# Kernel optimization log

Measured on AMD Instinct MI355X. Metric: run time of the kernel, lower is better.

## Reference

```python
import jax, jax.numpy as jnp
import numpy as np

D_MODEL, N_HEADS = 512, 8
HEAD_DIM = D_MODEL // N_HEADS
LN_EPS = 1e-5


def setup_inputs() -> dict:
    key = jax.random.key(0)
    ks = jax.random.split(key, 6)
    b, n = 8, 1024
    x = jax.random.normal(ks[0], (b, n, D_MODEL), dtype=jnp.float32)
    W_qkv = jax.random.normal(ks[1], (D_MODEL, 3 * D_MODEL), dtype=jnp.float32) * (1.0 / np.sqrt(D_MODEL))
    b_qkv = jnp.zeros((3 * D_MODEL,), dtype=jnp.float32)
    reattn_w = jax.random.normal(ks[2], (N_HEADS, N_HEADS), dtype=jnp.float32)
    ln_g = jnp.ones((N_HEADS,), dtype=jnp.float32)
    ln_b = jnp.zeros((N_HEADS,), dtype=jnp.float32)
    W_out = jax.random.normal(ks[3], (D_MODEL, D_MODEL), dtype=jnp.float32) * (1.0 / np.sqrt(D_MODEL))
    b_out = jnp.zeros((D_MODEL,), dtype=jnp.float32)
    return {"x": x, "W_qkv": W_qkv, "b_qkv": b_qkv, "reattn_w": reattn_w,
            "ln_g": ln_g, "ln_b": ln_b, "W_out": W_out, "b_out": b_out}


def reference(x, W_qkv, b_qkv, reattn_w, ln_g, ln_b, W_out, b_out):
    b, n, _ = x.shape
    scale = jnp.float32(HEAD_DIM ** -0.5)  # lsa=False -> non-trainable constant
    qkv = x @ W_qkv + b_qkv                                  # (b, n, 3*d_model)
    q, k, v = jnp.split(qkv, 3, axis=-1)
    def to_heads(t):  # b n (h d) -> b h n d
        return t.reshape(b, n, N_HEADS, HEAD_DIM).transpose(0, 2, 1, 3)
    q, k, v = to_heads(q), to_heads(k), to_heads(v)
    scores = jnp.einsum('bhid,bhjd->bhij', q, k) * scale      # (b, h, n, n)
    attn = jax.nn.softmax(scores, axis=-1)
    # cross-head re-attention mix
    attn = jnp.einsum('bhij,hk->bkij', attn, reattn_w)
    # LayerNorm over the head axis (axis=1)
    mu = jnp.mean(attn, axis=1, keepdims=True)
    var = jnp.var(attn, axis=1, keepdims=True)
    attn = (attn - mu) * jax.lax.rsqrt(var + LN_EPS)
    attn = attn * ln_g[None, :, None, None] + ln_b[None, :, None, None]
    out = jnp.einsum('bhij,bhjd->bhid', attn, v)              # (b, h, n, d)
    out = out.transpose(0, 2, 1, 3).reshape(b, n, D_MODEL)    # b n (h d)
    out = out @ W_out + b_out
    return (out, attn)
```

## Files before the change

### kernel.cpp

```cpp
#include <hip/hip_runtime.h>
#include <hip/hip_bf16.h>

#define SCALE_ 0.125f
#define LN_EPS_ 1e-5f

typedef __attribute__((ext_vector_type(8))) short bf16x8;
typedef __attribute__((ext_vector_type(4))) float f32x4;

__device__ __forceinline__ ushort f2b(float f) {
  union { float f; unsigned u; } x; x.f = f;
  unsigned r = x.u + 0x7FFFu + ((x.u >> 16) & 1u);
  return (ushort)(r >> 16);
}
__device__ __forceinline__ unsigned cvtpk(float lo, float hi) {
  union { __hip_bfloat162 h; unsigned u; } x;
  x.h = __float22bfloat162_rn(make_float2(lo, hi));
  return x.u;
}

__device__ __forceinline__ f32x4 mfma16(bf16x8 a, bf16x8 b, f32x4 c) {
  return __builtin_amdgcn_mfma_f32_16x16x32_bf16(a, b, c, 0, 0, 0);
}

__device__ __forceinline__ void bar_lds() {
  asm volatile("s_waitcnt lgkmcnt(0)\n\ts_barrier" ::: "memory");
  __builtin_amdgcn_sched_barrier(0);
}

__global__ __launch_bounds__(256) void cast_transpose2(const float* __restrict__ srcA,
                                                       ushort* __restrict__ dstA,
                                                       const float* __restrict__ srcB,
                                                       ushort* __restrict__ dstB) {
  __shared__ ushort t[64][65];
  const int bid = blockIdx.x;
  const float* src;
  ushort* dst;
  int R, C, c0, r0;
  if (bid < 192) {
    src = srcA; dst = dstA; R = 512; C = 1536;
    c0 = (bid % 24) * 64; r0 = (bid / 24) * 64;
  } else {
    src = srcB; dst = dstB; R = 512; C = 512;
    int b2 = bid - 192;
    c0 = (b2 % 8) * 64; r0 = (b2 / 8) * 64;
  }
  const int tid = threadIdx.x;
  const int lr = tid >> 2, lc = (tid & 3) * 16;
#pragma unroll
  for (int u = 0; u < 4; ++u) {
    float4 v = *(const float4*)&src[(size_t)(r0 + lr) * C + c0 + lc + u * 4];
    t[lc + u * 4 + 0][lr] = f2b(v.x);
    t[lc + u * 4 + 1][lr] = f2b(v.y);
    t[lc + u * 4 + 2][lr] = f2b(v.z);
    t[lc + u * 4 + 3][lr] = f2b(v.w);
  }
  __syncthreads();
#pragma unroll
  for (int u = 0; u < 2; ++u) {
    bf16x8 o;
#pragma unroll
    for (int e = 0; e < 8; ++e) o[e] = (short)t[lr][lc + u * 8 + e];
    *(bf16x8*)&dst[(size_t)(c0 + lr) * R + r0 + lc + u * 8] = o;
  }
}

__global__ __launch_bounds__(256) void qkv_mfma(const float* __restrict__ x,
                                                const ushort* __restrict__ Wt,
                                                const float* __restrict__ bias,
                                                ushort* __restrict__ q,
                                                ushort* __restrict__ k,
                                                ushort* __restrict__ vt) {
  __shared__ ushort A[128][40];
  __shared__ ushort Bs[128][40];
  const int tid = threadIdx.x;
  const int bid = blockIdx.x;
  const int obid = (bid & 7) * 96 + (bid >> 3);
  const int n0 = (obid % 12) * 128;
  const int m0 = (obid / 12) * 128;
  const int lane = tid & 63, wid = tid >> 6;
  const int wr = wid >> 1, wc = wid & 1;
  const int lr = lane & 15, g4 = lane >> 4;
  const int sr = tid >> 1, sco = (tid & 1) * 16;
  f32x4 acc[4][4] = {};
  for (int k0 = 0; k0 < 512; k0 += 32) {
    {
      const float4* xs = (const float4*)&x[(size_t)(m0 + sr) * 512 + k0 + sco];
      float4 v0 = xs[0], v1 = xs[1], v2 = xs[2], v3 = xs[3];
      bf16x8 p0, p1;
      p0[0] = (short)f2b(v0.x); p0[1] = (short)f2b(v0.y);
      p0[2] = (short)f2b(v0.z); p0[3] = (short)f2b(v0.w);
      p0[4] = (short)f2b(v1.x); p0[5] = (short)f2b(v1.y);
      p0[6] = (short)f2b(v1.z); p0[7] = (short)f2b(v1.w);
      p1[0] = (short)f2b(v2.x); p1[1] = (short)f2b(v2.y);
      p1[2] = (short)f2b(v2.z); p1[3] = (short)f2b(v2.w);
      p1[4] = (short)f2b(v3.x); p1[5] = (short)f2b(v3.y);
      p1[6] = (short)f2b(v3.z); p1[7] = (short)f2b(v3.w);
      *(bf16x8*)&A[sr][sco] = p0;
      *(bf16x8*)&A[sr][sco + 8] = p1;
    }
    {
      const bf16x8* wp = (const bf16x8*)&Wt[(size_t)(n0 + sr) * 512 + k0 + sco];
      *(bf16x8*)&Bs[sr][sco] = wp[0];
      *(bf16x8*)&Bs[sr][sco + 8] = wp[1];
    }
    __syncthreads();
    bf16x8 af[4], bf[4];
#pragma unroll
    for (int mr = 0; mr < 4; ++mr) af[mr] = *(bf16x8*)&A[wr * 64 + mr * 16 + lr][g4 * 8];
#pragma unroll
    for (int nr = 0; nr < 4; ++nr) bf[nr] = *(bf16x8*)&Bs[wc * 64 + nr * 16 + lr][g4 * 8];
#pragma unroll
    for (int mr = 0; mr < 4; ++mr)
#pragma unroll
      for (int nr = 0; nr < 4; ++nr) acc[mr][nr] = mfma16(af[mr], bf[nr], acc[mr][nr]);
    __syncthreads();
  }
  const int part = n0 >> 9;
#pragma unroll
  for (int mr = 0; mr < 4; ++mr)
#pragma unroll
    for (int nr = 0; nr < 4; ++nr) {
      const int n = n0 + wc * 64 + nr * 16 + lr;
      const int h = (n & 511) >> 6, d = n & 63;
      const float bb = bias[n];
#pragma unroll
      for (int r = 0; r < 4; ++r) {
        int token = m0 + wr * 64 + mr * 16 + g4 * 4 + r;
        int bi = token >> 10, ii = token & 1023;
        ushort valb = f2b(acc[mr][nr][r] + bb);
        if (part == 0)
          q[(((size_t)(bi * 8 + h) * 1024 + ii) * 64) + d] = valb;
        else if (part == 1)
          k[(((size_t)(bi * 8 + h) * 1024 + ii) * 64) + d] = valb;
        else
          vt[((size_t)(bi * 8 + h) * 64 + d) * 1024 + ii] = valb;
      }
    }
}

__global__ __launch_bounds__(512, 2) void attn_fused(const ushort* __restrict__ q,
                                                     const ushort* __restrict__ k,
                                                     const ushort* __restrict__ vt,
                                                     const float* __restrict__ rw,
                                                     const float* __restrict__ ln_g,
                                                     const float* __restrict__ ln_b,
                                                     float* __restrict__ attn,
                                                     ushort* __restrict__ pv) {
  __shared__ float PM[8][32][36];
  __shared__ float wsh[64];
  __shared__ float gsh[8], bsh[8];

  const int tid = threadIdx.x;
  const int lane = tid & 63;
  const int h = tid >> 6;
  const int obid = ((blockIdx.x & 7) << 5) + (blockIdx.x >> 3);
  const int i0 = (obid & 31) * 32;
  const int b = obid >> 5;
  const int lr = lane & 15, g4 = lane >> 4;

  const int bh = b * 8 + h;
  const ushort* qh = q + ((size_t)bh * 1024 + i0) * 64;
  const ushort* kh = k + (size_t)bh * 65536;
  const ushort* vth = vt + (size_t)bh * 65536;

  if (tid < 64) wsh[tid] = rw[tid];
  if (tid < 8) { gsh[tid] = ln_g[tid]; bsh[tid] = ln_b[tid]; }

  bf16x8 qf[2][2];
#pragma unroll
  for (int ir = 0; ir < 2; ++ir)
#pragma unroll
    for (int ks = 0; ks < 2; ++ks)
      qf[ir][ks] = *(const bf16x8*)&qh[(size_t)(ir * 16 + lr) * 64 + ks * 32 + g4 * 8];

  float psum[2] = {0.f, 0.f};
  {
    bf16x8 kc[4], kn[4];
#pragma unroll
    for (int jr = 0; jr < 2; ++jr)
#pragma unroll
      for (int ks = 0; ks < 2; ++ks)
        kc[jr * 2 + ks] = *(const bf16x8*)&kh[(size_t)(jr * 16 + lr) * 64 + ks * 32 + g4 * 8];
    for (int jt = 0; jt < 32; ++jt) {
      const int j0n = ((jt + 1) & 31) * 32;
#pragma unroll
      for (int jr = 0; jr < 2; ++jr)
#pragma unroll
        for (int ks = 0; ks < 2; ++ks)
          kn[jr * 2 + ks] =
              *(const bf16x8*)&kh[(size_t)(j0n + jr * 16 + lr) * 64 + ks * 32 + g4 * 8];
      f32x4 sa[2][2] = {};
#pragma unroll
      for (int jr = 0; jr < 2; ++jr)
#pragma unroll
        for (int ir = 0; ir < 2; ++ir) {
          sa[jr][ir] = mfma16(kc[jr * 2 + 0], qf[ir][0], sa[jr][ir]);
          sa[jr][ir] = mfma16(kc[jr * 2 + 1], qf[ir][1], sa[jr][ir]);
        }
#pragma unroll
      for (int jr = 0; jr < 2; ++jr)
#pragma unroll
        for (int ir = 0; ir < 2; ++ir)
#pragma unroll
          for (int r = 0; r < 4; ++r) psum[ir] += __expf(sa[jr][ir][r] * SCALE_);
#pragma unroll
      for (int i = 0; i < 4; ++i) kc[i] = kn[i];
    }
  }
  float inv_[2];
#pragma unroll
  for (int ir = 0; ir < 2; ++ir) {
    float s = psum[ir];
    s += __shfl_xor(s, 16);
    s += __shfl_xor(s, 32);
    inv_[ir] = 1.0f / s;
  }

  f32x4 oaccT[4][2] = {};
  const int pair = tid & 1, chunk = tid >> 1;
  const int m_ii = chunk >> 3, m_jj = (chunk & 7) * 4;
  const int k2base = pair * 4;

  bf16x8 kc[4], kn[4];
#pragma unroll
  for (int jr = 0; jr < 2; ++jr)
#pragma unroll
    for (int ks = 0; ks < 2; ++ks)
      kc[jr * 2 + ks] = *(const bf16x8*)&kh[(size_t)(jr * 16 + lr) * 64 + ks * 32 + g4 * 8];

  for (int jt = 0; jt < 32; ++jt) {
    const int j0 = jt * 32;
    const int j0n = ((jt + 1) & 31) * 32;
#pragma unroll
    for (int jr = 0; jr < 2; ++jr)
#pragma unroll
      for (int ks = 0; ks < 2; ++ks)
        kn[jr * 2 + ks] =
            *(const bf16x8*)&kh[(size_t)(j0n + jr * 16 + lr) * 64 + ks * 32 + g4 * 8];

    f32x4 sa[2][2] = {};
#pragma unroll
    for (int jr = 0; jr < 2; ++jr)
#pragma unroll
      for (int ir = 0; ir < 2; ++ir) {
        sa[jr][ir] = mfma16(kc[jr * 2 + 0], qf[ir][0], sa[jr][ir]);
        sa[jr][ir] = mfma16(kc[jr * 2 + 1], qf[ir][1], sa[jr][ir]);
      }
#pragma unroll
    for (int jr = 0; jr < 2; ++jr)
#pragma unroll
      for (int ir = 0; ir < 2; ++ir) {
        f32x4 pw;
#pragma unroll
        for (int r = 0; r < 4; ++r) pw[r] = __expf(sa[jr][ir][r] * SCALE_) * inv_[ir];
        *(f32x4*)&PM[h][ir * 16 + lr][jr * 16 + g4 * 4] = pw;
      }

    bf16x8 vc[4];
#pragma unroll
    for (int dr = 0; dr < 4; ++dr)
      vc[dr] = *(const bf16x8*)&vth[(size_t)(dr * 16 + lr) * 1024 + j0 + g4 * 8];

    bar_lds();

    float4 ph[8];
#pragma unroll
    for (int h2 = 0; h2 < 8; ++h2) ph[h2] = *(const float4*)&PM[h2][m_ii][m_jj];
    float mixed[4][4];
#pragma unroll
    for (int k2l = 0; k2l < 4; ++k2l) {
      float a0 = 0.f, a1 = 0.f, a2 = 0.f, a3 = 0.f;
#pragma unroll
      for (int h2 = 0; h2 < 8; ++h2) {
        float w = wsh[h2 * 8 + k2base + k2l];
        a0 += ph[h2].x * w; a1 += ph[h2].y * w;
        a2 += ph[h2].z * w; a3 += ph[h2].w * w;
      }
      mixed[k2l][0] = a0; mixed[k2l][1] = a1; mixed[k2l][2] = a2; mixed[k2l][3] = a3;
    }
    float mu[4], rs_[4];
#pragma unroll
    for (int e = 0; e < 4; ++e) {
      float mp = mixed[0][e] + mixed[1][e] + mixed[2][e] + mixed[3][e];
      mu[e] = (mp + __shfl_xor(mp, 1)) * 0.125f;
    }
#pragma unroll
    for (int e = 0; e < 4; ++e) {
      float vp = 0.f;
#pragma unroll
      for (int k2l = 0; k2l < 4; ++k2l) {
        float d = mixed[k2l][e] - mu[e];
        vp += d * d;
      }
      float var = (vp + __shfl_xor(vp, 1)) * 0.125f;
      rs_[e] = rsqrtf(var + LN_EPS_);
    }
#pragma unroll
    for (int k2l = 0; k2l < 4; ++k2l) {
      int k2 = k2base + k2l;
      float g = gsh[k2], be = bsh[k2];
      f32x4 o;
      o[0] = (mixed[k2l][0] - mu[0]) * rs_[0] * g + be;
      o[1] = (mixed[k2l][1] - mu[1]) * rs_[1] * g + be;
      o[2] = (mixed[k2l][2] - mu[2]) * rs_[2] * g + be;
      o[3] = (mixed[k2l][3] - mu[3]) * rs_[3] * g + be;
      __builtin_nontemporal_store(
          o, (f32x4*)&attn[((size_t)(b * 8 + k2) << 20) + ((size_t)(i0 + m_ii) << 10) +
                           j0 + m_jj]);
      *(f32x4*)&PM[k2][m_ii][m_jj] = o;
    }

    bar_lds();

    bf16x8 pab[2];
#pragma unroll
    for (int ic = 0; ic < 2; ++ic) {
      const float* pr = &PM[h][ic * 16 + lr][g4 * 8];
      float4 p0 = *(const float4*)&pr[0];
      float4 p1 = *(const float4*)&pr[4];
      union { bf16x8 v; unsigned u[4]; } pk;
      pk.u[0] = cvtpk(p0.x, p0.y);
      pk.u[1] = cvtpk(p0.z, p0.w);
      pk.u[2] = cvtpk(p1.x, p1.y);
      pk.u[3] = cvtpk(p1.z, p1.w);
      pab[ic] = pk.v;
    }
#pragma unroll
    for (int dr = 0; dr < 4; ++dr) {
      oaccT[dr][0] = mfma16(vc[dr], pab[0], oaccT[dr][0]);
      oaccT[dr][1] = mfma16(vc[dr], pab[1], oaccT[dr][1]);
    }

#pragma unroll
    for (int i = 0; i < 4; ++i) kc[i] = kn[i];
  }

  ushort* po = pv + ((size_t)bh * 1024 + i0) * 64;
#pragma unroll
  for (int ic = 0; ic < 2; ++ic)
#pragma unroll
    for (int dr = 0; dr < 4; ++dr) {
      union { ushort4 s; unsigned u[2]; } o;
      o.u[0] = cvtpk(oaccT[dr][ic][0], oaccT[dr][ic][1]);
      o.u[1] = cvtpk(oaccT[dr][ic][2], oaccT[dr][ic][3]);
      *(ushort4*)&po[(size_t)(ic * 16 + lr) * 64 + dr * 16 + g4 * 4] = o.s;
    }
}

__global__ __launch_bounds__(256) void out_mfma(const ushort* __restrict__ pvb,
                                                const ushort* __restrict__ Wt,
                                                const float* __restrict__ bias,
                                                float* __restrict__ out) {
  __shared__ ushort A[128][40];
  __shared__ ushort Bs[128][40];
  const int tid = threadIdx.x;
  const int bid = blockIdx.x;
  const int obid = ((bid & 7) << 5) + (bid >> 3);
  const int n0 = (obid & 3) * 128;
  const int m0 = (obid >> 2) * 128;
  const int lane = tid & 63, wid = tid >> 6;
  const int wr = wid >> 1, wc = wid & 1;
  const int lr = lane & 15, g4 = lane >> 4;
  const int sr = tid >> 1, sco = (tid & 1) * 16;
  f32x4 acc[4][4] = {};
  for (int k0 = 0; k0 < 512; k0 += 32) {
    {
      int token = m0 + sr;
      int bi = token >> 10, ii = token & 1023;
      int f = k0 + sco;
      int hh = f >> 6, d = f & 63;
      const bf16x8* src =
          (const bf16x8*)&pvb[(((size_t)(bi * 8 + hh)) * 1024 + ii) * 64 + d];
      *(bf16x8*)&A[sr][sco] = src[0];
      *(bf16x8*)&A[sr][sco + 8] = src[1];
    }
    {
      const bf16x8* wp = (const bf16x8*)&Wt[(size_t)(n0 + sr) * 512 + k0 + sco];
      *(bf16x8*)&Bs[sr][sco] = wp[0];
      *(bf16x8*)&Bs[sr][sco + 8] = wp[1];
    }
    __syncthreads();
    bf16x8 af[4], bf[4];
#pragma unroll
    for (int mr = 0; mr < 4; ++mr) af[mr] = *(bf16x8*)&A[wr * 64 + mr * 16 + lr][g4 * 8];
#pragma unroll
    for (int nr = 0; nr < 4; ++nr) bf[nr] = *(bf16x8*)&Bs[wc * 64 + nr * 16 + lr][g4 * 8];
#pragma unroll
    for (int mr = 0; mr < 4; ++mr)
#pragma unroll
      for (int nr = 0; nr < 4; ++nr) acc[mr][nr] = mfma16(af[mr], bf[nr], acc[mr][nr]);
    __syncthreads();
  }
#pragma unroll
  for (int mr = 0; mr < 4; ++mr)
#pragma unroll
    for (int nr = 0; nr < 4; ++nr) {
      const int n = n0 + wc * 64 + nr * 16 + lr;
      const float bb = bias[n];
#pragma unroll
      for (int r = 0; r < 4; ++r) {
        int token = m0 + wr * 64 + mr * 16 + g4 * 4 + r;
        out[(size_t)token * 512 + n] = acc[mr][nr][r] + bb;
      }
    }
}

extern "C" void kernel_launch(void* const* d_in, const int* in_sizes, int n_in,
                              void* d_out, int out_size, void* d_ws, size_t ws_size,
                              hipStream_t stream) {
  const float* x    = (const float*)d_in[0];
  const float* Wqkv = (const float*)d_in[1];
  const float* bqkv = (const float*)d_in[2];
  const float* rw   = (const float*)d_in[3];
  const float* lng  = (const float*)d_in[4];
  const float* lnb  = (const float*)d_in[5];
  const float* Wout = (const float*)d_in[6];
  const float* bout = (const float*)d_in[7];

  float* out  = (float*)d_out;
  float* attn = (float*)d_out + 4194304;

  char* wsb = (char*)d_ws;
  ushort* q     = (ushort*)(wsb);
  ushort* k     = (ushort*)(wsb + (8u << 20));
  ushort* vt    = (ushort*)(wsb + (16u << 20));
  ushort* pvb   = (ushort*)(wsb + (24u << 20));
  ushort* Wqkvt = (ushort*)(wsb + (32u << 20));
  ushort* Woutt = (ushort*)(wsb + (33u << 20) + (1u << 19));

  cast_transpose2<<<dim3(256), 256, 0, stream>>>(Wqkv, Wqkvt, Wout, Woutt);
  qkv_mfma<<<dim3(768), 256, 0, stream>>>(x, Wqkvt, bqkv, q, k, vt);
  attn_fused<<<dim3(256), 512, 0, stream>>>(q, k, vt, rw, lng, lnb, attn, pvb);
  out_mfma<<<dim3(256), 256, 0, stream>>>(pvb, Woutt, bout, out);
}
```

Before: 170.7 us.

## Split attention into denominator kernel and single-wave cross-head attn_pv kernel

```diff
diff --git a/kernel.cpp b/kernel.cpp
--- a/kernel.cpp
+++ b/kernel.cpp
@@ -20,11 +20,6 @@
 
 __device__ __forceinline__ f32x4 mfma16(bf16x8 a, bf16x8 b, f32x4 c) {
   return __builtin_amdgcn_mfma_f32_16x16x32_bf16(a, b, c, 0, 0, 0);
-}
-
-__device__ __forceinline__ void bar_lds() {
-  asm volatile("s_waitcnt lgkmcnt(0)\n\ts_barrier" ::: "memory");
-  __builtin_amdgcn_sched_barrier(0);
 }
 
 __global__ __launch_bounds__(256) void cast_transpose2(const float* __restrict__ srcA,
@@ -138,33 +133,17 @@
     }
 }
 
-__global__ __launch_bounds__(512, 2) void attn_fused(const ushort* __restrict__ q,
-                                                     const ushort* __restrict__ k,
-                                                     const ushort* __restrict__ vt,
-                                                     const float* __restrict__ rw,
-                                                     const float* __restrict__ ln_g,
-                                                     const float* __restrict__ ln_b,
-                                                     float* __restrict__ attn,
-                                                     ushort* __restrict__ pv) {
-  __shared__ float PM[8][32][36];
-  __shared__ float wsh[64];
-  __shared__ float gsh[8], bsh[8];
-
-  const int tid = threadIdx.x;
-  const int lane = tid & 63;
-  const int h = tid >> 6;
-  const int obid = ((blockIdx.x & 7) << 5) + (blockIdx.x >> 3);
-  const int i0 = (obid & 31) * 32;
-  const int b = obid >> 5;
+__global__ __launch_bounds__(64) void denoms(const ushort* __restrict__ q,
+                                             const ushort* __restrict__ k,
+                                             float* __restrict__ invg) {
+  const int bid = blockIdx.x;
+  const int obid = ((bid & 7) << 8) + (bid >> 3);
+  const int bh = obid >> 5;
+  const int it = obid & 31;
+  const int lane = threadIdx.x;
   const int lr = lane & 15, g4 = lane >> 4;
-
-  const int bh = b * 8 + h;
-  const ushort* qh = q + ((size_t)bh * 1024 + i0) * 64;
+  const ushort* qh = q + ((size_t)bh * 1024 + it * 32) * 64;
   const ushort* kh = k + (size_t)bh * 65536;
-  const ushort* vth = vt + (size_t)bh * 65536;
-
-  if (tid < 64) wsh[tid] = rw[tid];
-  if (tid < 8) { gsh[tid] = ln_g[tid]; bsh[tid] = ln_b[tid]; }
 
   bf16x8 qf[2][2];
 #pragma unroll
@@ -174,177 +153,165 @@
       qf[ir][ks] = *(const bf16x8*)&qh[(size_t)(ir * 16 + lr) * 64 + ks * 32 + g4 * 8];
 
   float psum[2] = {0.f, 0.f};
-  {
-    bf16x8 kc[4], kn[4];
+  bf16x8 kc[4], kn[4];
+#pragma unroll
+  for (int jr = 0; jr < 2; ++jr)
+#pragma unroll
+    for (int ks = 0; ks < 2; ++ks)
+      kc[jr * 2 + ks] = *(const bf16x8*)&kh[(size_t)(jr * 16 + lr) * 64 + ks * 32 + g4 * 8];
+  for (int jt = 0; jt < 32; ++jt) {
+    const int j0n = ((jt + 1) & 31) * 32;
 #pragma unroll
     for (int jr = 0; jr < 2; ++jr)
 #pragma unroll
       for (int ks = 0; ks < 2; ++ks)
-        kc[jr * 2 + ks] = *(const bf16x8*)&kh[(size_t)(jr * 16 + lr) * 64 + ks * 32 + g4 * 8];
-    for (int jt = 0; jt < 32; ++jt) {
-      const int j0n = ((jt + 1) & 31) * 32;
-#pragma unroll
-      for (int jr = 0; jr < 2; ++jr)
-#pragma unroll
-        for (int ks = 0; ks < 2; ++ks)
-          kn[jr * 2 + ks] =
-              *(const bf16x8*)&kh[(size_t)(j0n + jr * 16 + lr) * 64 + ks * 32 + g4 * 8];
-      f32x4 sa[2][2] = {};
-#pragma unroll
-      for (int jr = 0; jr < 2; ++jr)
-#pragma unroll
-        for (int ir = 0; ir < 2; ++ir) {
-          sa[jr][ir] = mfma16(kc[jr * 2 + 0], qf[ir][0], sa[jr][ir]);
-          sa[jr][ir] = mfma16(kc[jr * 2 + 1], qf[ir][1], sa[jr][ir]);
-        }
-#pragma unroll
-      for (int jr = 0; jr < 2; ++jr)
-#pragma unroll
-        for (int ir = 0; ir < 2; ++ir)
-#pragma unroll
-          for (int r = 0; r < 4; ++r) psum[ir] += __expf(sa[jr][ir][r] * SCALE_);
-#pragma unroll
-      for (int i = 0; i < 4; ++i) kc[i] = kn[i];
-    }
-  }
-  float inv_[2];
+        kn[jr * 2 + ks] =
+            *(const bf16x8*)&kh[(size_t)(j0n + jr * 16 + lr) * 64 + ks * 32 + g4 * 8];
+    f32x4 sa[2][2] = {};
+#pragma unroll
+    for (int jr = 0; jr < 2; ++jr)
+#pragma unroll
+      for (int ir = 0; ir < 2; ++ir) {
+        sa[jr][ir] = mfma16(kc[jr * 2 + 0], qf[ir][0], sa[jr][ir]);
+        sa[jr][ir] = mfma16(kc[jr * 2 + 1], qf[ir][1], sa[jr][ir]);
+      }
+#pragma unroll
+    for (int jr = 0; jr < 2; ++jr)
+#pragma unroll
+      for (int ir = 0; ir < 2; ++ir)
+#pragma unroll
+        for (int r = 0; r < 4; ++r) psum[ir] += __expf(sa[jr][ir][r] * SCALE_);
+#pragma unroll
+    for (int i = 0; i < 4; ++i) kc[i] = kn[i];
+  }
 #pragma unroll
   for (int ir = 0; ir < 2; ++ir) {
     float s = psum[ir];
     s += __shfl_xor(s, 16);
     s += __shfl_xor(s, 32);
-    inv_[ir] = 1.0f / s;
-  }
-
-  f32x4 oaccT[4][2] = {};
-  const int pair = tid & 1, chunk = tid >> 1;
-  const int m_ii = chunk >> 3, m_jj = (chunk & 7) * 4;
-  const int k2base = pair * 4;
-
-  bf16x8 kc[4], kn[4];
-#pragma unroll
-  for (int jr = 0; jr < 2; ++jr)
+    psum[ir] = s;
+  }
+  if (lane < 16) {
+    invg[(size_t)bh * 1024 + it * 32 + lr] = 1.0f / psum[0];
+    invg[(size_t)bh * 1024 + it * 32 + 16 + lr] = 1.0f / psum[1];
+  }
+}
+
+__global__ __launch_bounds__(64, 1) void attn_pv(const ushort* __restrict__ q,
+                                                 const ushort* __restrict__ k,
+                                                 const ushort* __restrict__ vt,
+                                                 const float* __restrict__ rw,
+                                                 const float* __restrict__ ln_g,
+                                                 const float* __restrict__ ln_b,
+                                                 const float* __restrict__ invg,
+                                                 float* __restrict__ attn,
+                                                 ushort* __restrict__ pv) {
+  __shared__ float pl[4][16][36];
+  const int bid = blockIdx.x;
+  const int obid = ((bid & 7) << 7) + (bid >> 3);
+  const int b = obid >> 7;
+  const int rem = obid & 127;
+  const int i0 = (rem >> 1) * 16;
+  const int hf = rem & 1;
+  const int lane = threadIdx.x;
+  const int lr = lane & 15, g4 = lane >> 4;
+
+  float wv[64];
+#pragma unroll
+  for (int i = 0; i < 64; ++i) wv[i] = rw[i];
+  float gv[8], bv[8];
+#pragma unroll
+  for (int i = 0; i < 8; ++i) { gv[i] = ln_g[i]; bv[i] = ln_b[i]; }
+
+  bf16x8 qf[8][2];
+  float inv_[8];
+#pragma unroll
+  for (int h = 0; h < 8; ++h) {
+    const ushort* qh = q + ((size_t)(b * 8 + h) * 1024 + i0) * 64;
 #pragma unroll
     for (int ks = 0; ks < 2; ++ks)
-      kc[jr * 2 + ks] = *(const bf16x8*)&kh[(size_t)(jr * 16 + lr) * 64 + ks * 32 + g4 * 8];
-
-  for (int jt = 0; jt < 32; ++jt) {
-    const int j0 = jt * 32;
-    const int j0n = ((jt + 1) & 31) * 32;
-#pragma unroll
-    for (int jr = 0; jr < 2; ++jr)
-#pragma unroll
-      for (int ks = 0; ks < 2; ++ks)
-        kn[jr * 2 + ks] =
-            *(const bf16x8*)&kh[(size_t)(j0n + jr * 16 + lr) * 64 + ks * 32 + g4 * 8];
-
-    f32x4 sa[2][2] = {};
-#pragma unroll
-    for (int jr = 0; jr < 2; ++jr)
-#pragma unroll
-      for (int ir = 0; ir < 2; ++ir) {
-        sa[jr][ir] = mfma16(kc[jr * 2 + 0], qf[ir][0], sa[jr][ir]);
-        sa[jr][ir] = mfma16(kc[jr * 2 + 1], qf[ir][1], sa[jr][ir]);
-      }
-#pragma unroll
-    for (int jr = 0; jr < 2; ++jr)
-#pragma unroll
-      for (int ir = 0; ir < 2; ++ir) {
-        f32x4 pw;
-#pragma unroll
-        for (int r = 0; r < 4; ++r) pw[r] = __expf(sa[jr][ir][r] * SCALE_) * inv_[ir];
-        *(f32x4*)&PM[h][ir * 16 + lr][jr * 16 + g4 * 4] = pw;
-      }
-
-    bf16x8 vc[4];
-#pragma unroll
-    for (int dr = 0; dr < 4; ++dr)
-      vc[dr] = *(const bf16x8*)&vth[(size_t)(dr * 16 + lr) * 1024 + j0 + g4 * 8];
-
-    bar_lds();
-
-    float4 ph[8];
-#pragma unroll
-    for (int h2 = 0; h2 < 8; ++h2) ph[h2] = *(const float4*)&PM[h2][m_ii][m_jj];
-    float mixed[4][4];
-#pragma unroll
-    for (int k2l = 0; k2l < 4; ++k2l) {
-      float a0 = 0.f, a1 = 0.f, a2 = 0.f, a3 = 0.f;
-#pragma unroll
-      for (int h2 = 0; h2 < 8; ++h2) {
-        float w = wsh[h2 * 8 + k2base + k2l];
-        a0 += ph[h2].x * w; a1 += ph[h2].y * w;
-        a2 += ph[h2].z * w; a3 += ph[h2].w * w;
-      }
-      mixed[k2l][0] = a0; mixed[k2l][1] = a1; mixed[k2l][2] = a2; mixed[k2l][3] = a3;
-    }
-    float mu[4], rs_[4];
-#pragma unroll
-    for (int e = 0; e < 4; ++e) {
-      float mp = mixed[0][e] + mixed[1][e] + mixed[2][e] + mixed[3][e];
-      mu[e] = (mp + __shfl_xor(mp, 1)) * 0.125f;
-    }
-#pragma unroll
-    for (int e = 0; e < 4; ++e) {
-      float vp = 0.f;
-#pragma unroll
-      for (int k2l = 0; k2l < 4; ++k2l) {
-        float d = mixed[k2l][e] - mu[e];
-        vp += d * d;
-      }
-      float var = (vp + __shfl_xor(vp, 1)) * 0.125f;
-      rs_[e] = rsqrtf(var + LN_EPS_);
-    }
-#pragma unroll
-    for (int k2l = 0; k2l < 4; ++k2l) {
-      int k2 = k2base + k2l;
-      float g = gsh[k2], be = bsh[k2];
-      f32x4 o;
-      o[0] = (mixed[k2l][0] - mu[0]) * rs_[0] * g + be;
-      o[1] = (mixed[k2l][1] - mu[1]) * rs_[1] * g + be;
-      o[2] = (mixed[k2l][2] - mu[2]) * rs_[2] * g + be;
-      o[3] = (mixed[k2l][3] - mu[3]) * rs_[3] * g + be;
-      __builtin_nontemporal_store(
-          o, (f32x4*)&attn[((size_t)(b * 8 + k2) << 20) + ((size_t)(i0 + m_ii) << 10) +
-                           j0 + m_jj]);
-      *(f32x4*)&PM[k2][m_ii][m_jj] = o;
-    }
-
-    bar_lds();
-
-    bf16x8 pab[2];
-#pragma unroll
-    for (int ic = 0; ic < 2; ++ic) {
-      const float* pr = &PM[h][ic * 16 + lr][g4 * 8];
-      float4 p0 = *(const float4*)&pr[0];
-      float4 p1 = *(const float4*)&pr[4];
-      union { bf16x8 v; unsigned u[4]; } pk;
-      pk.u[0] = cvtpk(p0.x, p0.y);
-      pk.u[1] = cvtpk(p0.z, p0.w);
-      pk.u[2] = cvtpk(p1.x, p1.y);
-      pk.u[3] = cvtpk(p1.z, p1.w);
-      pab[ic] = pk.v;
-    }
-#pragma unroll
-    for (int dr = 0; dr < 4; ++dr) {
-      oaccT[dr][0] = mfma16(vc[dr], pab[0], oaccT[dr][0]);
-      oaccT[dr][1] = mfma16(vc[dr], pab[1], oaccT[dr][1]);
-    }
-
-#pragma unroll
-    for (int i = 0; i < 4; ++i) kc[i] = kn[i];
-  }
-
-  ushort* po = pv + ((size_t)bh * 1024 + i0) * 64;
-#pragma unroll
-  for (int ic = 0; ic < 2; ++ic)
-#pragma unroll
-    for (int dr = 0; dr < 4; ++dr) {
+      qf[h][ks] = *(const bf16x8*)&qh[(size_t)lr * 64 + ks * 32 + g4 * 8];
+    inv_[h] = invg[(size_t)(b * 8 + h) * 1024 + i0 + lr];
+  }
+
+  f32x4 oaccT[4][4] = {};
+
+  for (int t = 0; t < 32; ++t) {
+    const int j0 = t * 32;
+#pragma unroll
+    for (int jr = 0; jr < 2; ++jr) {
+      const int jb = j0 + jr * 16;
+      f32x4 mixed[8] = {};
+#pragma unroll
+      for (int h = 0; h < 8; ++h) {
+        const ushort* kh = k + (size_t)(b * 8 + h) * 65536;
+        bf16x8 k0v = *(const bf16x8*)&kh[(size_t)(jb + lr) * 64 + g4 * 8];
+        bf16x8 k1v = *(const bf16x8*)&kh[(size_t)(jb + lr) * 64 + 32 + g4 * 8];
+        f32x4 sa = {};
+        sa = mfma16(k0v, qf[h][0], sa);
+        sa = mfma16(k1v, qf[h][1], sa);
+        f32x4 p;
+#pragma unroll
+        for (int r = 0; r < 4; ++r) p[r] = __expf(sa[r] * SCALE_) * inv_[h];
+#pragma unroll
+        for (int k2 = 0; k2 < 8; ++k2) mixed[k2] += p * wv[h * 8 + k2];
+      }
+      f32x4 mu = mixed[0];
+#pragma unroll
+      for (int k2 = 1; k2 < 8; ++k2) mu += mixed[k2];
+      mu *= 0.125f;
+      f32x4 var = {};
+#pragma unroll
+      for (int k2 = 0; k2 < 8; ++k2) { f32x4 d = mixed[k2] - mu; var += d * d; }
+      var *= 0.125f;
+      f32x4 rs;
+#pragma unroll
+      for (int r = 0; r < 4; ++r) rs[r] = rsqrtf(var[r] + LN_EPS_);
+#pragma unroll
+      for (int k2 = 0; k2 < 8; ++k2)
+        mixed[k2] = (mixed[k2] - mu) * rs * gv[k2] + bv[k2];
+
+      if ((jb >> 9) == hf) {
+#pragma unroll
+        for (int k2 = 0; k2 < 8; ++k2)
+          *(f32x4*)&attn[((size_t)(b * 8 + k2) << 20) + ((size_t)(i0 + lr) << 10) +
+                         jb + g4 * 4] = mixed[k2];
+      }
+#pragma unroll
+      for (int hl = 0; hl < 4; ++hl)
+        *(f32x4*)&pl[hl][lr][jr * 16 + g4 * 4] = mixed[hf * 4 + hl];
+    }
+
+#pragma unroll
+    for (int hl = 0; hl < 4; ++hl) {
+      const float* pr = &pl[hl][lr][g4 * 8];
+      f32x4 p0 = *(const f32x4*)&pr[0];
+      f32x4 p1 = *(const f32x4*)&pr[4];
+      union { bf16x8 v; unsigned u[4]; } pb;
+      pb.u[0] = cvtpk(p0[0], p0[1]);
+      pb.u[1] = cvtpk(p0[2], p0[3]);
+      pb.u[2] = cvtpk(p1[0], p1[1]);
+      pb.u[3] = cvtpk(p1[2], p1[3]);
+      const ushort* vh = vt + (size_t)(b * 8 + hf * 4 + hl) * 65536;
+#pragma unroll
+      for (int dt = 0; dt < 4; ++dt) {
+        bf16x8 vf = *(const bf16x8*)&vh[(size_t)(dt * 16 + lr) * 1024 + j0 + g4 * 8];
+        oaccT[hl][dt] = mfma16(vf, pb.v, oaccT[hl][dt]);
+      }
+    }
+  }
+
+#pragma unroll
+  for (int hl = 0; hl < 4; ++hl) {
+    ushort* po = pv + ((size_t)(b * 8 + hf * 4 + hl) * 1024 + i0) * 64;
+#pragma unroll
+    for (int dt = 0; dt < 4; ++dt) {
       union { ushort4 s; unsigned u[2]; } o;
-      o.u[0] = cvtpk(oaccT[dr][ic][0], oaccT[dr][ic][1]);
-      o.u[1] = cvtpk(oaccT[dr][ic][2], oaccT[dr][ic][3]);
-      *(ushort4*)&po[(size_t)(ic * 16 + lr) * 64 + dr * 16 + g4 * 4] = o.s;
-    }
+      o.u[0] = cvtpk(oaccT[hl][dt][0], oaccT[hl][dt][1]);
+      o.u[1] = cvtpk(oaccT[hl][dt][2], oaccT[hl][dt][3]);
+      *(ushort4*)&po[(size_t)lr * 64 + dt * 16 + g4 * 4] = o.s;
+    }
+  }
 }
 
 __global__ __launch_bounds__(256) void out_mfma(const ushort* __restrict__ pvb,
@@ -427,9 +394,11 @@
   ushort* pvb   = (ushort*)(wsb + (24u << 20));
   ushort* Wqkvt = (ushort*)(wsb + (32u << 20));
   ushort* Woutt = (ushort*)(wsb + (33u << 20) + (1u << 19));
+  float*  invg  = (float*)(wsb + (34u << 20));
 
   cast_transpose2<<<dim3(256), 256, 0, stream>>>(Wqkv, Wqkvt, Wout, Woutt);
   qkv_mfma<<<dim3(768), 256, 0, stream>>>(x, Wqkvt, bqkv, q, k, vt);
-  attn_fused<<<dim3(256), 512, 0, stream>>>(q, k, vt, rw, lng, lnb, attn, pvb);
+  denoms<<<dim3(2048), 64, 0, stream>>>(q, k, invg);
+  attn_pv<<<dim3(1024), 64, 0, stream>>>(q, k, vt, rw, lng, lnb, invg, attn, pvb);
   out_mfma<<<dim3(256), 256, 0, stream>>>(pvb, Woutt, bout, out);
 }
```

Result: slower. 452.3 us (+164.9%).
